# Kernel tuning notes

Hardware: AMD Instinct MI355X
Metric: run time of the kernel (lower is better)

The kernel has to match this reference:

```python
import jax, jax.numpy as jnp
import numpy as np

T = 2048          # total (flattened) tokens
HID = 4096
NQ = 32           # query heads
NKV = 8           # kv heads
D = 128           # head_dim
B = 4             # dllm block length (block-sparse attention block)
WIN = 1024        # sliding window
EPS = 1e-6


def _rope_tables():
    # standard RoPE cos/sin tables, half-dim frequencies duplicated
    inv_freq = 1.0 / (10000.0 ** (np.arange(0, D, 2, dtype=np.float32) / D))
    pos = np.arange(T, dtype=np.float32)
    freqs = np.outer(pos, inv_freq)                     # [T, D/2]
    emb = np.concatenate([freqs, freqs], axis=-1)       # [T, D]
    return jnp.asarray(np.cos(emb)), jnp.asarray(np.sin(emb))


def setup_inputs() -> dict:
    key = jax.random.key(0)
    ks = jax.random.split(key, 4)
    cos, sin = _rope_tables()
    return {
        "hidden_states": jax.random.normal(ks[0], (T, HID), jnp.float32),
        "cos": cos,
        "sin": sin,
        "w_qkv": jax.random.normal(ks[1], (HID, (NQ + 2 * NKV) * D), jnp.float32) * (HID ** -0.5),
        "q_norm_w": jnp.ones((D,), jnp.float32),
        "k_norm_w": jnp.ones((D,), jnp.float32),
        "w_o": jax.random.normal(ks[2], (NQ * D, HID), jnp.float32) * ((NQ * D) ** -0.5),
    }


def _rmsnorm(x, w):
    # per-head RMSNorm over last dim (head_dim)
    var = jnp.mean(jnp.square(x), axis=-1, keepdims=True)
    return x * jax.lax.rsqrt(var + EPS) * w


def _rotate_half(x):
    x1, x2 = jnp.split(x, 2, axis=-1)
    return jnp.concatenate([-x2, x1], axis=-1)


def reference(hidden_states, cos, sin, w_qkv, q_norm_w, k_norm_w, w_o):
    # fused QKV projection on flattened tokens [T, HID]
    qkv = hidden_states @ w_qkv                                  # [T, (NQ+2NKV)*D]
    q, k, v = jnp.split(qkv, [NQ * D, (NQ + NKV) * D], axis=-1)
    q = q.reshape(T, NQ, D)
    k = k.reshape(T, NKV, D)
    v = v.reshape(T, NKV, D)

    # per-head QK RMSNorm
    q = _rmsnorm(q, q_norm_w)
    k = _rmsnorm(k, k_norm_w)

    # RoPE
    c = cos[:, None, :]
    s = sin[:, None, :]
    q = q * c + _rotate_half(q) * s
    k = k * c + _rotate_half(k) * s

    # GQA: expand kv heads to query heads
    groups = NQ // NKV
    k = jnp.repeat(k, groups, axis=1)                            # [T, NQ, D]
    v = jnp.repeat(v, groups, axis=1)

    # block-sparse (dLLM block-causal) + sliding-window mask:
    # token q attends to token j iff block(j) <= block(q) (full bidirectional
    # attention within a dllm block, causal across blocks) AND j is within
    # the sliding window.
    pos = jnp.arange(T)
    qb = pos // B
    allowed = (qb[None, :] <= qb[:, None]) & ((pos[:, None] - pos[None, :]) < WIN)

    scale = D ** -0.5
    scores = jnp.einsum("qhd,khd->hqk", q, k) * scale            # [NQ, T, T]
    scores = jnp.where(allowed[None, :, :], scores, jnp.float32(-1e30))
    probs = jax.nn.softmax(scores, axis=-1)
    attn = jnp.einsum("hqk,khd->qhd", probs, v)                   # [T, NQ, D]

    out = attn.reshape(T, NQ * D) @ w_o                           # [T, HID]
    return out
```

## Files before the change

### kernel.cpp

```cpp
#include <hip/hip_runtime.h>
#include <hip/hip_bf16.h>

typedef unsigned short u16;
typedef __attribute__((ext_vector_type(8))) short bf16x8;
typedef __attribute__((ext_vector_type(4))) float f32x4;
typedef __attribute__((ext_vector_type(8))) u16 u16x8;
typedef __attribute__((ext_vector_type(4))) u16 u16x4;

#define T_SEQ 2048
#define HID 4096
#define NQ 32
#define NKV 8
#define DH 128
#define WIN 1024

__device__ __forceinline__ u16 f2bf(float f) {
  union { float f; unsigned int u; } v; v.f = f;
  unsigned int u = v.u;
  unsigned int r = (u + 0x7FFFu + ((u >> 16) & 1u)) >> 16;
  return (u16)r;
}
__device__ __forceinline__ float bf2f(u16 b) {
  union { unsigned int u; float f; } v; v.u = ((unsigned int)b) << 16;
  return v.f;
}

__device__ __forceinline__ void gload16(const void* g, void* l) {
  __builtin_amdgcn_global_load_lds(
      (const __attribute__((address_space(1))) unsigned int*)g,
      (__attribute__((address_space(3))) unsigned int*)l, 16, 0, 0);
}

__global__ __launch_bounds__(256) void f32_to_bf16(const float* __restrict__ in,
                                                   u16* __restrict__ out, int n) {
  int i = (blockIdx.x * 256 + threadIdx.x) * 8;
  if (i >= n) return;
  float4 a = *(const float4*)(in + i);
  float4 b = *(const float4*)(in + i + 4);
  u16x8 r;
  r[0] = f2bf(a.x); r[1] = f2bf(a.y); r[2] = f2bf(a.z); r[3] = f2bf(a.w);
  r[4] = f2bf(b.x); r[5] = f2bf(b.y); r[6] = f2bf(b.z); r[7] = f2bf(b.w);
  *(u16x8*)(out + i) = r;
}

__global__ __launch_bounds__(256) void transpose_f32_to_bf16(const float* __restrict__ in,
                                                             u16* __restrict__ out,
                                                             int R, int C) {
  __shared__ float tile[64][65];
  int c0 = blockIdx.x * 64, r0 = blockIdx.y * 64;
  int tx = threadIdx.x, ty = threadIdx.y;
#pragma unroll
  for (int i = 0; i < 64; i += 16) {
    float4 v = *(const float4*)(in + (size_t)(r0 + ty + i) * C + c0 + tx * 4);
    tile[ty + i][tx * 4 + 0] = v.x;
    tile[ty + i][tx * 4 + 1] = v.y;
    tile[ty + i][tx * 4 + 2] = v.z;
    tile[ty + i][tx * 4 + 3] = v.w;
  }
  __syncthreads();
#pragma unroll
  for (int i = 0; i < 64; i += 16) {
    u16x4 o;
#pragma unroll
    for (int j = 0; j < 4; ++j) o[j] = f2bf(tile[tx * 4 + j][ty + i]);
    *(u16x4*)(out + (size_t)(c0 + ty + i) * R + r0 + tx * 4) = o;
  }
}

__global__ __launch_bounds__(256) void v_transpose(const u16* __restrict__ Vn,
                                                   u16* __restrict__ Vt) {
  __shared__ u16 tile[64][68];
  int tx = threadIdx.x & 15, ty = threadIdx.x >> 4;
  int t0 = blockIdx.x * 64, dh0 = blockIdx.y * 64;
#pragma unroll
  for (int i = 0; i < 64; i += 16) {
    u16x4 v = *(const u16x4*)(Vn + (size_t)(t0 + ty + i) * 1024 + dh0 + tx * 4);
    tile[ty + i][tx * 4 + 0] = v[0];
    tile[ty + i][tx * 4 + 1] = v[1];
    tile[ty + i][tx * 4 + 2] = v[2];
    tile[ty + i][tx * 4 + 3] = v[3];
  }
  __syncthreads();
#pragma unroll
  for (int i = 0; i < 64; i += 16) {
    u16x4 o;
#pragma unroll
    for (int j = 0; j < 4; ++j) o[j] = tile[tx * 4 + j][ty + i];
    *(u16x4*)(Vt + (size_t)(dh0 + ty + i) * 2048 + t0 + tx * 4) = o;
  }
}

template <int NF, bool BF16OUT>
__global__ __launch_bounds__(512, 2) void gemm_1w(const u16* __restrict__ A,
                                                  const u16* __restrict__ Bt,
                                                  void* __restrict__ Cv,
                                                  int N, int K, int NT) {
  constexpr int HN = NF * 16;
  constexpr int BN = 4 * HN;
  constexpr int NB = BN / 64;
  __shared__ u16 lsA[2][16384];
  __shared__ u16 lsB[3][BN * 64];
  const int tid = threadIdx.x;
  const int lane = tid & 63, w = tid >> 6;
  const int wm = w >> 1, wn = w & 1;
  const int l15 = lane & 15, l4 = lane >> 4;

  const int nwg = gridDim.x;
  const int cpx = nwg >> 3;
  const int bid = blockIdx.x;
  const int swz = (bid & 7) * cpx + (bid >> 3);
  const int bm = (swz & 7) * 256;
  const int bn = (swz >> 3) * BN;

  auto stageA = [&](int unit, int slot, int kt) {
    int r = tid >> 3, cp = tid & 7;
    int scp = cp ^ (r & 7);
    gload16(A + (size_t)(bm + unit * 64 + r) * K + kt * 64 + scp * 8,
            (char*)lsA[slot] + (unit * 512 + tid) * 16);
  };
  auto stageB = [&](int unit, int slot, int kt) {
    int r = tid >> 3, cp = tid & 7;
    int scp = cp ^ (r & 7);
    gload16(Bt + (size_t)(bn + unit * 64 + r) * K + kt * 64 + scp * 8,
            (char*)lsB[slot] + (unit * 512 + tid) * 16);
  };
  auto rdA = [&](int slot, int mf, int ks) -> bf16x8 {
    int r = wm * 64 + mf * 16 + l15;
    int ch = (ks * 4 + l4) ^ (r & 7);
    return *(const bf16x8*)(lsA[slot] + r * 64 + ch * 8);
  };
  auto rdB = [&](int slot, int nf, int ks) -> bf16x8 {
    int r = wn * 2 * HN + nf * 16 + l15;
    int ch = (ks * 4 + l4) ^ (r & 7);
    return *(const bf16x8*)(lsB[slot] + r * 64 + ch * 8);
  };

#define WAIT_NB() do { if constexpr (NB == 3) asm volatile("s_waitcnt vmcnt(3)" ::: "memory"); \
                       else                   asm volatile("s_waitcnt vmcnt(2)" ::: "memory"); } while (0)

  f32x4 acc[4][2 * NF] = {};
  bf16x8 afA[4][2], bfr[2 * NF][2];

  stageA(0, 0, 0); stageA(1, 0, 0); stageA(2, 0, 0); stageA(3, 0, 0);
#pragma unroll
  for (int u = 0; u < NB; ++u) stageB(u, 0, 0);
#pragma unroll
  for (int u = 0; u < NB; ++u) stageB(u, 1, 1);
  WAIT_NB();
  __builtin_amdgcn_s_barrier();

  for (int t = 0; t < NT; ++t) {
    const int sA = t & 1, sB = t % 3;
    const int ktA = (t + 1 < NT) ? t + 1 : NT - 1;
    const int ktB = (t + 2 < NT) ? t + 2 : NT - 1;

#pragma unroll
    for (int mf = 0; mf < 4; ++mf)
#pragma unroll
      for (int ks = 0; ks < 2; ++ks) afA[mf][ks] = rdA(sA, mf, ks);
#pragma unroll
    for (int nf = 0; nf < 2 * NF; ++nf)
#pragma unroll
      for (int ks = 0; ks < 2; ++ks) bfr[nf][ks] = rdB(sB, nf, ks);
    stageA(0, (t + 1) & 1, ktA); stageA(1, (t + 1) & 1, ktA);
    stageA(2, (t + 1) & 1, ktA); stageA(3, (t + 1) & 1, ktA);
#pragma unroll
    for (int u = 0; u < NB; ++u) stageB(u, (t + 2) % 3, ktB);
    asm volatile("s_waitcnt lgkmcnt(0)" ::: "memory");
    __builtin_amdgcn_sched_barrier(0);
    __builtin_amdgcn_s_setprio(1);
#pragma unroll
    for (int mf = 0; mf < 4; ++mf)
#pragma unroll
      for (int nf = 0; nf < 2 * NF; ++nf) {
        acc[mf][nf] = __builtin_amdgcn_mfma_f32_16x16x32_bf16(afA[mf][0], bfr[nf][0], acc[mf][nf], 0, 0, 0);
        acc[mf][nf] = __builtin_amdgcn_mfma_f32_16x16x32_bf16(afA[mf][1], bfr[nf][1], acc[mf][nf], 0, 0, 0);
      }
    __builtin_amdgcn_s_setprio(0);
    WAIT_NB();
    __builtin_amdgcn_s_barrier();
  }

  asm volatile("s_waitcnt vmcnt(0)" ::: "memory");

#pragma unroll
  for (int mi = 0; mi < 4; ++mi)
#pragma unroll
    for (int ni = 0; ni < 2 * NF; ++ni) {
      int row = bm + wm * 64 + mi * 16 + l4 * 4;
      int col = bn + wn * 2 * HN + ni * 16 + l15;
      if constexpr (BF16OUT) {
        u16* dst = (u16*)Cv;
#pragma unroll
        for (int j = 0; j < 4; ++j)
          dst[(size_t)(row + j) * N + col] = f2bf(acc[mi][ni][j]);
      } else {
        float* p = (float*)Cv + (size_t)row * N + col;
        p[0] = acc[mi][ni][0];
        p[(size_t)N] = acc[mi][ni][1];
        p[2 * (size_t)N] = acc[mi][ni][2];
        p[3 * (size_t)N] = acc[mi][ni][3];
      }
    }
#undef WAIT_NB
}

__global__ __launch_bounds__(256) void rope_kernel(const u16* __restrict__ qkv,
                                                   const float* __restrict__ cosb,
                                                   const float* __restrict__ sinb,
                                                   const float* __restrict__ qw,
                                                   const float* __restrict__ kw,
                                                   u16* __restrict__ Qo,
                                                   u16* __restrict__ Ko,
                                                   u16* __restrict__ Vn) {
  int wid = threadIdx.x >> 6, lane = threadIdx.x & 63;
  int item = blockIdx.x * 4 + wid;
  int t = item / 48, hid = item % 48;
  const u16* x = qkv + (size_t)t * 6144 + hid * 128;
  float x1 = bf2f(x[lane]), x2 = bf2f(x[lane + 64]);
  if (hid < NQ + NKV) {
    float ss = x1 * x1 + x2 * x2;
    for (int off = 32; off; off >>= 1) ss += __shfl_xor(ss, off);
    float inv = rsqrtf(ss * (1.0f / 128.0f) + 1e-6f);
    const float* wn = (hid < NQ) ? qw : kw;
    float n1 = x1 * inv * wn[lane], n2 = x2 * inv * wn[lane + 64];
    float c1 = cosb[t * 128 + lane], s1 = sinb[t * 128 + lane];
    float c2 = cosb[t * 128 + lane + 64], s2 = sinb[t * 128 + lane + 64];
    float o1 = n1 * c1 - n2 * s1;
    float o2 = n2 * c2 + n1 * s2;
    if (hid < NQ) {
      const float scale = 0.08838834764831845f;
      u16* q = Qo + ((size_t)hid * T_SEQ + t) * 128;
      q[lane] = f2bf(o1 * scale); q[lane + 64] = f2bf(o2 * scale);
    } else {
      int h = hid - NQ;
      u16* k = Ko + ((size_t)h * T_SEQ + t) * 128;
      k[lane] = f2bf(o1); k[lane + 64] = f2bf(o2);
    }
  } else {
    int h = hid - (NQ + NKV);
    u16* vn = Vn + (size_t)t * 1024 + h * 128;
    vn[lane] = x[lane];
    vn[lane + 64] = x[lane + 64];
  }
}

__global__ __launch_bounds__(256) void attn_kernel(const u16* __restrict__ Q,
                                                   const u16* __restrict__ Kb,
                                                   const u16* __restrict__ Vt,
                                                   u16* __restrict__ O) {
  __shared__ u16 kls[2][64 * 128];
  __shared__ u16 vls[2][128 * 64];
  __shared__ u16 plds[4][16 * 72];

  const int tid = threadIdx.x;
  const int lane = tid & 63, w = tid >> 6;
  const int l15 = lane & 15, l4 = lane >> 4;
  const int h = blockIdx.x;
  const int q0 = blockIdx.y * 64;
  const int wq0 = q0 + w * 16;
  const int kvh = h >> 2;

  bf16x8 qf[4];
  {
    const u16* qrow = Q + ((size_t)h * T_SEQ + (wq0 + l15)) * DH;
    for (int ks = 0; ks < 4; ++ks)
      qf[ks] = *(const bf16x8*)(qrow + ks * 32 + l4 * 8);
  }

  f32x4 acc[8] = {};
  float m = -1e30f, lsum = 0.f;

  int ks0 = q0 - (WIN - 1); if (ks0 < 0) ks0 = 0;
  ks0 &= ~63;
  const int kend = q0;

  auto stage = [&](int b, int k0) {
#pragma unroll
    for (int c = 0; c < 4; ++c) {
      int base = w * 4096 + c * 1024;
      int idx = base / 16 + lane;
      {
        int row = idx >> 4;
        int col = (idx & 15) ^ (row & 7);
        gload16(Kb + ((size_t)kvh * T_SEQ + k0 + row) * DH + col * 8,
                (char*)kls[b] + base);
      }
      {
        int d = idx >> 3;
        int ch = (idx & 7) ^ (d & 7);
        gload16(Vt + ((size_t)kvh * DH + d) * T_SEQ + k0 + ch * 8,
                (char*)vls[b] + base);
      }
    }
  };

  stage(0, ks0);
  int buf = 0;
  for (int k0 = ks0; k0 <= kend; k0 += 64) {
    bool more = (k0 + 64 <= kend);
    if (more) stage(buf ^ 1, k0 + 64);
    if (more) { asm volatile("s_waitcnt vmcnt(8)" ::: "memory"); }
    else      { asm volatile("s_waitcnt vmcnt(0)" ::: "memory"); }
    __builtin_amdgcn_s_barrier();
    __builtin_amdgcn_sched_barrier(0);

    if (k0 <= wq0 + 15 && k0 + 63 >= wq0 - (WIN - 1)) {
      f32x4 st[4];
      __builtin_amdgcn_s_setprio(1);
#pragma unroll
      for (int kh = 0; kh < 4; ++kh) {
        f32x4 s = {};
        int row = kh * 16 + l15;
        const char* kb = (const char*)kls[buf] + row * 256;
#pragma unroll
        for (int ks = 0; ks < 4; ++ks) {
          int chunk = (ks * 4 + l4) ^ (row & 7);
          bf16x8 kf = *(const bf16x8*)(kb + chunk * 16);
          s = __builtin_amdgcn_mfma_f32_16x16x32_bf16(kf, qf[ks], s, 0, 0, 0);
        }
        st[kh] = s;
      }
      __builtin_amdgcn_s_setprio(0);
      const int q = wq0 + l15;
      float pv[4][4];
      float mx = -3e38f;
      if (k0 + 64 <= wq0 && k0 >= wq0 - 1008) {
#pragma unroll
        for (int kh = 0; kh < 4; ++kh)
#pragma unroll
          for (int i = 0; i < 4; ++i) {
            pv[kh][i] = st[kh][i];
            mx = fmaxf(mx, pv[kh][i]);
          }
      } else {
#pragma unroll
        for (int kh = 0; kh < 4; ++kh)
#pragma unroll
          for (int i = 0; i < 4; ++i) {
            int k = k0 + kh * 16 + l4 * 4 + i;
            bool ok = ((k >> 2) <= (q >> 2)) && (q - k < WIN);
            float s = ok ? st[kh][i] : -3e38f;
            pv[kh][i] = s;
            mx = fmaxf(mx, s);
          }
      }
      mx = fmaxf(mx, __shfl_xor(mx, 16));
      mx = fmaxf(mx, __shfl_xor(mx, 32));
      if (!__all(mx <= m + 8.f)) {
        float mn = fmaxf(m, mx);
        float sc = __expf(m - mn);
        m = mn;
        lsum *= sc;
#pragma unroll
        for (int nt = 0; nt < 8; ++nt)
#pragma unroll
          for (int i = 0; i < 4; ++i) acc[nt][i] *= sc;
      }
      float rs = 0.f;
#pragma unroll
      for (int kh = 0; kh < 4; ++kh)
#pragma unroll
        for (int i = 0; i < 4; ++i) {
          float p = __expf(pv[kh][i] - m);
          pv[kh][i] = p;
          rs += p;
        }
      rs += __shfl_xor(rs, 16);
      rs += __shfl_xor(rs, 32);
      lsum += rs;
      u16* pw = plds[w];
#pragma unroll
      for (int kh = 0; kh < 4; ++kh) {
        unsigned int d0 = (unsigned int)f2bf(pv[kh][0]) | ((unsigned int)f2bf(pv[kh][1]) << 16);
        unsigned int d1 = (unsigned int)f2bf(pv[kh][2]) | ((unsigned int)f2bf(pv[kh][3]) << 16);
        *(unsigned int*)(pw + l15 * 72 + kh * 16 + l4 * 4) = d0;
        *(unsigned int*)(pw + l15 * 72 + kh * 16 + l4 * 4 + 2) = d1;
      }
      bf16x8 pf0 = *(const bf16x8*)(pw + l15 * 72 + l4 * 8);
      bf16x8 pf1 = *(const bf16x8*)(pw + l15 * 72 + 32 + l4 * 8);
      __builtin_amdgcn_s_setprio(1);
#pragma unroll
      for (int nt = 0; nt < 8; ++nt) {
        int d = nt * 16 + l15;
        int ch0 = l4 ^ (d & 7);
        int ch1 = (4 + l4) ^ (d & 7);
        bf16x8 vf0 = *(const bf16x8*)((const char*)vls[buf] + d * 128 + ch0 * 16);
        bf16x8 vf1 = *(const bf16x8*)((const char*)vls[buf] + d * 128 + ch1 * 16);
        acc[nt] = __builtin_amdgcn_mfma_f32_16x16x32_bf16(vf0, pf0, acc[nt], 0, 0, 0);
        acc[nt] = __builtin_amdgcn_mfma_f32_16x16x32_bf16(vf1, pf1, acc[nt], 0, 0, 0);
      }
      __builtin_amdgcn_s_setprio(0);
    }
    __builtin_amdgcn_sched_barrier(0);
    __builtin_amdgcn_s_barrier();
    buf ^= 1;
  }

  float inv = 1.0f / lsum;
#pragma unroll
  for (int nt = 0; nt < 8; ++nt) {
    u16x4 o;
#pragma unroll
    for (int i = 0; i < 4; ++i) o[i] = f2bf(acc[nt][i] * inv);
    *(u16x4*)(O + (size_t)(wq0 + l15) * (NQ * DH) + h * DH + nt * 16 + l4 * 4) = o;
  }
}

extern "C" void kernel_launch(void* const* d_in, const int* in_sizes, int n_in,
                              void* d_out, int out_size, void* d_ws, size_t ws_size,
                              hipStream_t stream) {
  const float* hidden = (const float*)d_in[0];
  const float* cosb   = (const float*)d_in[1];
  const float* sinb   = (const float*)d_in[2];
  const float* w_qkv  = (const float*)d_in[3];
  const float* qnw    = (const float*)d_in[4];
  const float* knw    = (const float*)d_in[5];
  const float* w_o    = (const float*)d_in[6];
  float* out = (float*)d_out;
  char* ws = (char*)d_ws;

  u16*   wqkvT  = (u16*)(ws);
  u16*   hid_bf = (u16*)(ws + ((size_t)48 << 20));
  u16*   qkv_bf = (u16*)(ws + ((size_t)64 << 20));
  u16*   vn_bf  = (u16*)(ws + ((size_t)88 << 20));
  u16*   q_bf   = (u16*)(ws + ((size_t)112 << 20));
  u16*   k_bf   = (u16*)(ws + ((size_t)128 << 20));
  u16*   vt_bf  = (u16*)(ws + ((size_t)132 << 20));
  u16*   attn_bf= (u16*)(ws + ((size_t)48 << 20));
  u16*   woT    = (u16*)(ws);

  f32_to_bf16<<<4096, 256, 0, stream>>>(hidden, hid_bf, T_SEQ * HID);
  transpose_f32_to_bf16<<<dim3(96, 64), dim3(16, 16), 0, stream>>>(w_qkv, wqkvT, HID, 6144);
  gemm_1w<3, true><<<256, 512, 0, stream>>>(hid_bf, wqkvT, qkv_bf, 6144, HID, 64);
  transpose_f32_to_bf16<<<dim3(64, 64), dim3(16, 16), 0, stream>>>(w_o, woT, NQ * DH, HID);
  rope_kernel<<<(T_SEQ * 48) / 4, 256, 0, stream>>>(qkv_bf, cosb, sinb, qnw, knw, q_bf, k_bf, vn_bf);
  v_transpose<<<dim3(32, 16), 256, 0, stream>>>(vn_bf, vt_bf);
  attn_kernel<<<dim3(NQ, T_SEQ / 64), 256, 0, stream>>>(q_bf, k_bf, vt_bf, attn_bf);
  gemm_1w<2, false><<<256, 512, 0, stream>>>(attn_bf, woT, out, HID, NQ * DH, 64);
}
```

Measured before the change: 311.5 us.

## Add 128x128-tile output GEMM and switch attention softmax to exp2

Adds a new output-projection GEMM kernel with 128x128 tiles, 4 waves, 2 blocks per CU, and a triple-buffered B / double-buffered A LDS pipeline, and launches it with 512 blocks in place of the previous 256-block, 512-thread kernel. The attention softmax now folds log2(e) into the Q scale so it can use the hardware exp2 instruction, and widens the lazy-rescale threshold to match the new base. The bf16 packing of probabilities uses the native v_cvt_pk_bf16_f32 instruction instead of manual rounding. The aims are better occupancy and latency hiding in the output GEMM and fewer ALU instructions in the softmax, with a small rounding difference from the packed conversion.

```diff
diff --git a/kernel.cpp b/kernel.cpp
--- a/kernel.cpp
+++ b/kernel.cpp
@@ -203,6 +203,107 @@
       }
     }
 #undef WAIT_NB
+}
+
+__global__ __launch_bounds__(256, 2) void gemm_1wh(const u16* __restrict__ A,
+                                                   const u16* __restrict__ Bt,
+                                                   float* __restrict__ C,
+                                                   int N, int K, int NT) {
+  __shared__ u16 lsA[2][8192];
+  __shared__ u16 lsB[3][8192];
+  const int tid = threadIdx.x;
+  const int lane = tid & 63, w = tid >> 6;
+  const int wm = w >> 1, wn = w & 1;
+  const int l15 = lane & 15, l4 = lane >> 4;
+
+  const int nwg = gridDim.x;
+  const int cpx = nwg >> 3;
+  const int bid = blockIdx.x;
+  const int swz = (bid & 7) * cpx + (bid >> 3);
+  const int bm = (swz & 15) * 128;
+  const int bn = (swz >> 4) * 128;
+
+  auto stageA = [&](int unit, int slot, int kt) {
+    int r = unit * 32 + (tid >> 3), cp = tid & 7;
+    int scp = cp ^ (r & 7);
+    gload16(A + (size_t)(bm + r) * K + kt * 64 + scp * 8,
+            (char*)lsA[slot] + (unit * 256 + tid) * 16);
+  };
+  auto stageB = [&](int unit, int slot, int kt) {
+    int r = unit * 32 + (tid >> 3), cp = tid & 7;
+    int scp = cp ^ (r & 7);
+    gload16(Bt + (size_t)(bn + r) * K + kt * 64 + scp * 8,
+            (char*)lsB[slot] + (unit * 256 + tid) * 16);
+  };
+  auto rdA = [&](int slot, int mf, int ks) -> bf16x8 {
+    int r = wm * 64 + mf * 16 + l15;
+    int ch = (ks * 4 + l4) ^ (r & 7);
+    return *(const bf16x8*)(lsA[slot] + r * 64 + ch * 8);
+  };
+  auto rdB = [&](int slot, int nf, int ks) -> bf16x8 {
+    int r = wn * 64 + nf * 16 + l15;
+    int ch = (ks * 4 + l4) ^ (r & 7);
+    return *(const bf16x8*)(lsB[slot] + r * 64 + ch * 8);
+  };
+
+  f32x4 acc[4][4] = {};
+  bf16x8 afA[4][2], bfr[4][2];
+
+#pragma unroll
+  for (int u = 0; u < 4; ++u) stageA(u, 0, 0);
+#pragma unroll
+  for (int u = 0; u < 4; ++u) stageB(u, 0, 0);
+#pragma unroll
+  for (int u = 0; u < 4; ++u) stageB(u, 1, 1);
+  asm volatile("s_waitcnt vmcnt(4)" ::: "memory");
+  __builtin_amdgcn_s_barrier();
+
+  for (int t = 0; t < NT; ++t) {
+    const int sA = t & 1, sB = t % 3;
+    const int ktA = (t + 1 < NT) ? t + 1 : NT - 1;
+    const int ktB = (t + 2 < NT) ? t + 2 : NT - 1;
+
+#pragma unroll
+    for (int mf = 0; mf < 4; ++mf)
+#pragma unroll
+      for (int ks = 0; ks < 2; ++ks) afA[mf][ks] = rdA(sA, mf, ks);
+#pragma unroll
+    for (int nf = 0; nf < 4; ++nf)
+#pragma unroll
+      for (int ks = 0; ks < 2; ++ks) bfr[nf][ks] = rdB(sB, nf, ks);
+#pragma unroll
+    for (int u = 0; u < 4; ++u) stageA(u, (t + 1) & 1, ktA);
+#pragma unroll
+    for (int u = 0; u < 4; ++u) stageB(u, (t + 2) % 3, ktB);
+    asm volatile("s_waitcnt lgkmcnt(0)" ::: "memory");
+    __builtin_amdgcn_sched_barrier(0);
+    __builtin_amdgcn_s_setprio(1);
+#pragma unroll
+    for (int mf = 0; mf < 4; ++mf)
+#pragma unroll
+      for (int nf = 0; nf < 4; ++nf) {
+        acc[mf][nf] = __builtin_amdgcn_mfma_f32_16x16x32_bf16(afA[mf][0], bfr[nf][0], acc[mf][nf], 0, 0, 0);
+        acc[mf][nf] = __builtin_amdgcn_mfma_f32_16x16x32_bf16(afA[mf][1], bfr[nf][1], acc[mf][nf], 0, 0, 0);
+      }
+    __builtin_amdgcn_s_setprio(0);
+    asm volatile("s_waitcnt vmcnt(4)" ::: "memory");
+    __builtin_amdgcn_s_barrier();
+  }
+
+  asm volatile("s_waitcnt vmcnt(0)" ::: "memory");
+
+#pragma unroll
+  for (int mi = 0; mi < 4; ++mi)
+#pragma unroll
+    for (int ni = 0; ni < 4; ++ni) {
+      int row = bm + wm * 64 + mi * 16 + l4 * 4;
+      int col = bn + wn * 64 + ni * 16 + l15;
+      float* p = C + (size_t)row * N + col;
+      p[0] = acc[mi][ni][0];
+      p[(size_t)N] = acc[mi][ni][1];
+      p[2 * (size_t)N] = acc[mi][ni][2];
+      p[3 * (size_t)N] = acc[mi][ni][3];
+    }
 }
 
 __global__ __launch_bounds__(256) void rope_kernel(const u16* __restrict__ qkv,
@@ -229,7 +330,7 @@
     float o1 = n1 * c1 - n2 * s1;
     float o2 = n2 * c2 + n1 * s2;
     if (hid < NQ) {
-      const float scale = 0.08838834764831845f;
+      const float scale = 0.08838834764831845f * 1.44269504088896341f;
       u16* q = Qo + ((size_t)hid * T_SEQ + t) * 128;
       q[lane] = f2bf(o1 * scale); q[lane + 64] = f2bf(o2 * scale);
     } else {
@@ -347,9 +448,9 @@
       }
       mx = fmaxf(mx, __shfl_xor(mx, 16));
       mx = fmaxf(mx, __shfl_xor(mx, 32));
-      if (!__all(mx <= m + 8.f)) {
+      if (!__all(mx <= m + 11.5f)) {
         float mn = fmaxf(m, mx);
-        float sc = __expf(m - mn);
+        float sc = __builtin_amdgcn_exp2f(m - mn);
         m = mn;
         lsum *= sc;
 #pragma unroll
@@ -362,7 +463,7 @@
       for (int kh = 0; kh < 4; ++kh)
 #pragma unroll
         for (int i = 0; i < 4; ++i) {
-          float p = __expf(pv[kh][i] - m);
+          float p = __builtin_amdgcn_exp2f(pv[kh][i] - m);
           pv[kh][i] = p;
           rs += p;
         }
@@ -372,8 +473,9 @@
       u16* pw = plds[w];
 #pragma unroll
       for (int kh = 0; kh < 4; ++kh) {
-        unsigned int d0 = (unsigned int)f2bf(pv[kh][0]) | ((unsigned int)f2bf(pv[kh][1]) << 16);
-        unsigned int d1 = (unsigned int)f2bf(pv[kh][2]) | ((unsigned int)f2bf(pv[kh][3]) << 16);
+        unsigned int d0, d1;
+        asm("v_cvt_pk_bf16_f32 %0, %1, %2" : "=v"(d0) : "v"(pv[kh][0]), "v"(pv[kh][1]));
+        asm("v_cvt_pk_bf16_f32 %0, %1, %2" : "=v"(d1) : "v"(pv[kh][2]), "v"(pv[kh][3]));
         *(unsigned int*)(pw + l15 * 72 + kh * 16 + l4 * 4) = d0;
         *(unsigned int*)(pw + l15 * 72 + kh * 16 + l4 * 4 + 2) = d1;
       }
@@ -437,5 +539,5 @@
   rope_kernel<<<(T_SEQ * 48) / 4, 256, 0, stream>>>(qkv_bf, cosb, sinb, qnw, knw, q_bf, k_bf, vn_bf);
   v_transpose<<<dim3(32, 16), 256, 0, stream>>>(vn_bf, vt_bf);
   attn_kernel<<<dim3(NQ, T_SEQ / 64), 256, 0, stream>>>(q_bf, k_bf, vt_bf, attn_bf);
-  gemm_1w<2, false><<<256, 512, 0, stream>>>(attn_bf, woT, out, HID, NQ * DH, 64);
-}
+  gemm_1wh<<<512, 256, 0, stream>>>(attn_bf, woT, out, HID, NQ * DH, 64);
+}
```

After: 303.8 us. 2.5% less time.
